# Optimization experiments

Hardware: AMD Instinct MI355X
Metric: run time of the kernel (lower is better)

## Reference

```python
import jax, jax.numpy as jnp
import numpy as np
import math

B, N, E, H = 32, 2000, 128, 8
D = E // H
NEG = -1e9
LN_EPS = 1e-5

def setup_inputs() -> dict:
    key = jax.random.key(0)
    ks = jax.random.split(key, 20)
    s = 1.0 / math.sqrt(E)
    inp = {
        'decoder_state': jax.random.normal(ks[0], (B, E), jnp.float32),
        'node_embeddings': jax.random.normal(ks[1], (B, N, E), jnp.float32),
        'mask': jax.random.randint(ks[2], (B, N), 0, 2, jnp.int32),
        'edge_weights': jax.random.uniform(ks[3], (B, N, N), jnp.float32),
        'visited': jax.random.randint(ks[4], (B, N), 0, 2).astype(bool),
        'prev_node': jax.random.randint(ks[5], (B,), 0, N, jnp.int64 if jax.config.jax_enable_x64 else jnp.int32),
        'all_visited': jax.random.randint(ks[6], (B,), 0, 2).astype(bool),
        'Wq': jax.random.uniform(ks[7], (E, E), jnp.float32, -s, s),
        'bq': jnp.zeros((E,), jnp.float32),
        'Wk': jax.random.uniform(ks[8], (E, E), jnp.float32, -s, s),
        'bk': jnp.zeros((E,), jnp.float32),
        'Wv': jax.random.uniform(ks[9], (E, E), jnp.float32, -s, s),
        'bv': jnp.zeros((E,), jnp.float32),
        'Wo': jax.random.uniform(ks[10], (E, E), jnp.float32, -s, s),
        'bo': jnp.zeros((E,), jnp.float32),
        'Wp': jax.random.uniform(ks[11], (E, E), jnp.float32, -s, s),
        'bp': jnp.zeros((E,), jnp.float32),
        'ln_g': jnp.ones((E,), jnp.float32),
        'ln_b': jnp.zeros((E,), jnp.float32),
        'shortcut_bonus': jnp.float32(5.0),
        'revisit_penalty': jnp.float32(-0.5),
    }
    return inp

def _forward(decoder_state, node_embeddings, edge_weights, Wq, bq, Wk, bk, Wv, bv, Wo, bo, Wp, bp, ln_g, ln_b, shortcut_bonus, revisit_penalty, mask, visited, prev_node, all_visited):
    # single-query MHA: q [B,1,E], kv [B,N,E]
    q = (decoder_state @ Wq + bq).reshape(B, H, 1, D)            # q_len=1
    k = (node_embeddings @ Wk + bk).reshape(B, N, H, D).transpose(0, 2, 1, 3)
    v = (node_embeddings @ Wv + bv).reshape(B, N, H, D).transpose(0, 2, 1, 3)
    att = jnp.einsum('bhqd,bhkd->bhqk', q, k) / math.sqrt(D)     # [B,H,1,N]
    att = jnp.where(mask[:, None, None, :] == 0, NEG, att)
    w = jax.nn.softmax(att, axis=-1)
    ctx = jnp.einsum('bhqk,bhkd->bhqd', w, v).transpose(0, 2, 1, 3).reshape(B, E)
    ctx = ctx @ Wo + bo
    # dropout in eval mode = identity; LayerNorm
    mu = jnp.mean(ctx, axis=-1, keepdims=True)
    var = jnp.mean((ctx - mu) ** 2, axis=-1, keepdims=True)
    nrm = (ctx - mu) / jnp.sqrt(var + LN_EPS) * ln_g + ln_b
    logits = nrm @ Wp + bp                                        # [B,E]
    scores = jnp.einsum('be,bne->bn', logits, node_embeddings)    # [B,N]
    # vectorized per-batch loop semantics
    not_all = ~all_visited                                        # [B]
    scores = jnp.where(not_all[:, None] & visited, revisit_penalty, scores)
    bidx = jnp.arange(B)
    direct = edge_weights[bidx, prev_node, 0]                     # [B]
    via = edge_weights[bidx, prev_node, :] + edge_weights[:, :, 0]  # [B,N]
    sav = (direct[:, None] - via) / direct[:, None]
    bonus = jnp.where(all_visited[:, None] & (via < direct[:, None]), shortcut_bonus * sav, 0.0)
    return scores + bonus

def reference(decoder_state, node_embeddings, mask, edge_weights, visited, prev_node, all_visited, Wq, bq, Wk, bk, Wv, bv, Wo, bo, Wp, bp, ln_g, ln_b, shortcut_bonus, revisit_penalty):
    return _forward(decoder_state, node_embeddings, edge_weights, Wq, bq, Wk, bk, Wv, bv, Wo, bo, Wp, bp, ln_g, ln_b, shortcut_bonus, revisit_penalty, mask, visited, prev_node, all_visited)
```

## Files before the change

kernel.cpp:

```cpp
#include <hip/hip_runtime.h>
#include <cstddef>

#define BB 32
#define NN 2000
#define EE 128
#define HH 8
#define DD 16
#define NCH 32
#define CHN 64
#define NEGV (-1e9f)

typedef __attribute__((ext_vector_type(8))) short short8v;
typedef __attribute__((ext_vector_type(4))) float f32x4;

__device__ __forceinline__ short f2bf(float f) {
  unsigned u = __float_as_uint(f);
  unsigned r = (u + 0x7FFFu + ((u >> 16) & 1u)) >> 16;
  return (short)r;
}
__device__ __forceinline__ float bf2f(short s) {
  return __uint_as_float(((unsigned)(unsigned short)s) << 16);
}


__global__ __launch_bounds__(256) void k_fused(
    const float* __restrict__ ds, const float* __restrict__ ne, const int* __restrict__ mask,
    const float* __restrict__ Wq, const float* __restrict__ bq,
    const float* __restrict__ Wk, const float* __restrict__ bk,
    short* __restrict__ pctx, float* __restrict__ pm, float* __restrict__ ps) {
  const int cpair = blockIdx.x, b = blockIdx.y, t = threadIdx.x;

  __shared__ float ds_s[EE], q_s[EE];
  __shared__ float redq[256];
  __shared__ __align__(16) short qk_sub[16 * EE];
  __shared__ float qbk_s[HH];
  __shared__ __align__(16) short ne_sub[CHN * EE];
  __shared__ __align__(16) short wT[16 * 72];
  __shared__ float att_s[HH * 66];
  __shared__ int mask_s[CHN];

  const int baseA = (2 * cpair) * CHN;
  const int baseB = baseA + CHN;
  const int cntB = (NN - baseB < CHN) ? (NN - baseB) : CHN;
  const int nrow = t >> 4, oct = t & 15;

  float4 pA[8];
#pragma unroll
  for (int i = 0; i < 4; ++i) {
    const int n = i * 16 + nrow;
    const float4* sA = (const float4*)(ne + ((size_t)b * NN + baseA + n) * EE + oct * 8);
    pA[2 * i] = sA[0]; pA[2 * i + 1] = sA[1];
  }
  int maskA_r = 0;
  if (t < CHN) maskA_r = mask[b * NN + baseA + t];
  if (t < EE) ds_s[t] = ds[b * EE + t];
  __builtin_amdgcn_sched_barrier(0);
  __syncthreads();

  const int o = t & 127, half = t >> 7;
  {
    const int c0 = half * 64;
    float a0 = 0.f, a1 = 0.f, a2 = 0.f, a3 = 0.f;
    for (int c = c0; c < c0 + 64; c += 4) {
      a0 = fmaf(ds_s[c],     Wq[(c)     * EE + o], a0);
      a1 = fmaf(ds_s[c + 1], Wq[(c + 1) * EE + o], a1);
      a2 = fmaf(ds_s[c + 2], Wq[(c + 2) * EE + o], a2);
      a3 = fmaf(ds_s[c + 3], Wq[(c + 3) * EE + o], a3);
    }
    redq[t] = (a0 + a1) + (a2 + a3);
  }
  __syncthreads();
  if (t < 128) q_s[t] = bq[t] + redq[t] + redq[t + 128];
  __syncthreads();

#pragma unroll
  for (int k = 0; k < 4; ++k) {
    const int f = t + k * 256;
    const int h = f >> 7, e = f & 127;
    const float4* wk4 = (const float4*)(Wk + e * EE + h * DD);
    const float4* q4 = (const float4*)(q_s + h * DD);
    float s = 0.f;
#pragma unroll
    for (int i = 0; i < 4; ++i) {
      const float4 w = wk4[i], q = q4[i];
      s += w.x * q.x + w.y * q.y + w.z * q.z + w.w * q.w;
    }
    qk_sub[((e >> 4) * 4 + (h >> 2)) * 64 + (h & 3) * 16 + (e & 15)] = f2bf(s);
  }
  for (int f = t; f < 512; f += 256) {
    const int eb = f >> 6, r = f & 63;
    ((int*)(qk_sub + eb * 256 + 128))[r] = 0;
  }
  if (t < HH) {
    float s = 0.f;
#pragma unroll
    for (int d = 0; d < DD; ++d) s += q_s[t * DD + d] * bk[t * DD + d];
    qbk_s[t] = s;
  }
  for (int f = t; f < 288; f += 256) ((int*)(wT + 8 * 72))[f] = 0;

  if (t < CHN) mask_s[t] = maskA_r;
#pragma unroll
  for (int i = 0; i < 4; ++i) {
    const int n = i * 16 + nrow;
    short8v s8;
    s8[0] = f2bf(pA[2 * i].x);     s8[1] = f2bf(pA[2 * i].y);
    s8[2] = f2bf(pA[2 * i].z);     s8[3] = f2bf(pA[2 * i].w);
    s8[4] = f2bf(pA[2 * i + 1].x); s8[5] = f2bf(pA[2 * i + 1].y);
    s8[6] = f2bf(pA[2 * i + 1].z); s8[7] = f2bf(pA[2 * i + 1].w);
    *(short8v*)(ne_sub + ((oct >> 1) * 16 + (n >> 2)) * 64 + (n & 3) * 16 + (oct & 1) * 8) = s8;
  }

  float4 pB[8];
#pragma unroll
  for (int i = 0; i < 4; ++i) {
    const int n = i * 16 + nrow;
    if (n < cntB) {
      const float4* sB = (const float4*)(ne + ((size_t)b * NN + baseB + n) * EE + oct * 8);
      pB[2 * i] = sB[0]; pB[2 * i + 1] = sB[1];
    } else {
      pB[2 * i] = make_float4(0.f, 0.f, 0.f, 0.f);
      pB[2 * i + 1] = make_float4(0.f, 0.f, 0.f, 0.f);
    }
  }
  int maskB_r = 0;
  if (t < CHN) maskB_r = (t < cntB) ? mask[b * NN + baseB + t] : 0;
  __builtin_amdgcn_sched_barrier(0);
  __syncthreads();

  const int w = t >> 6;
  const int l = t & 63;
  const int g = l >> 4;
  const int l15 = l & 15;

#pragma unroll 1
  for (int cc = 0; cc < 2; ++cc) {
    const int ci = 2 * cpair + cc;

    {
      f32x4 qacc = {0.f, 0.f, 0.f, 0.f};
      const int rn = w * 16 + l15;
#pragma unroll
      for (int ks = 0; ks < 4; ++ks) {
        const int eb = ks * 2 + (g >> 1), elo = (g & 1) * 8;
        short8v a = *(const short8v*)(qk_sub + (eb * 4 + (l15 >> 2)) * 64 + (l15 & 3) * 16 + elo);
        short8v bb = *(const short8v*)(ne_sub + (eb * 16 + (rn >> 2)) * 64 + (rn & 3) * 16 + elo);
        qacc = __builtin_amdgcn_mfma_f32_16x16x32_bf16(a, bb, qacc, 0, 0, 0);
      }
      if (g < 2) {
#pragma unroll
        for (int r = 0; r < 4; ++r) {
          const int h = g * 4 + r;
          att_s[h * 66 + rn] = mask_s[rn] ? (qacc[r] + qbk_s[h]) * 0.25f : NEGV;
        }
      }
    }
    __syncthreads();

    {
      const int h = t >> 5, l32 = t & 31;
      const float a0 = att_s[h * 66 + l32], a1 = att_s[h * 66 + l32 + 32];
      float mx = fmaxf(a0, a1);
#pragma unroll
      for (int k = 16; k >= 1; k >>= 1) mx = fmaxf(mx, __shfl_xor(mx, k, 32));
      const float w0 = mask_s[l32] ? expf(a0 - mx) : 0.f;
      const float w1 = mask_s[l32 + 32] ? expf(a1 - mx) : 0.f;
      const short s0 = f2bf(w0), s1 = f2bf(w1);
      float sm = bf2f(s0) + bf2f(s1);
#pragma unroll
      for (int k = 16; k >= 1; k >>= 1) sm += __shfl_xor(sm, k, 32);
      wT[h * 72 + l32] = s0;
      wT[h * 72 + l32 + 32] = s1;
      if (l32 == 0) {
        pm[(b * NCH + ci) * HH + h] = mx;
        ps[(b * NCH + ci) * HH + h] = sm;
      }
    }
    __syncthreads();

    {
      f32x4 pacc0 = {0.f, 0.f, 0.f, 0.f}, pacc1 = {0.f, 0.f, 0.f, 0.f};
#pragma unroll
      for (int ks = 0; ks < 2; ++ks) {
        short8v a = *(const short8v*)(wT + l15 * 72 + ks * 32 + g * 8);
#pragma unroll
        for (int ti = 0; ti < 2; ++ti) {
          const int e = (2 * w + ti) * 16 + l15;
          short8v bb;
#pragma unroll
          for (int j = 0; j < 8; ++j) {
            const int n = ks * 32 + g * 8 + j;
            bb[j] = ne_sub[((e >> 4) * 16 + (n >> 2)) * 64 + (n & 3) * 16 + (e & 15)];
          }
          if (ti == 0) pacc0 = __builtin_amdgcn_mfma_f32_16x16x32_bf16(a, bb, pacc0, 0, 0, 0);
          else         pacc1 = __builtin_amdgcn_mfma_f32_16x16x32_bf16(a, bb, pacc1, 0, 0, 0);
        }
      }
      if (g < 2) {
        short* dst = pctx + ((size_t)(b * NCH + ci) * HH) * EE;
#pragma unroll
        for (int r = 0; r < 4; ++r) {
          const int h = g * 4 + r;
          dst[h * EE + (2 * w) * 16 + l15]     = f2bf(pacc0[r]);
          dst[h * EE + (2 * w + 1) * 16 + l15] = f2bf(pacc1[r]);
        }
      }
    }

    if (cc == 0) {
      __syncthreads();
      if (t < CHN) mask_s[t] = maskB_r;
#pragma unroll
      for (int i = 0; i < 4; ++i) {
        const int n = i * 16 + nrow;
        short8v s8;
        s8[0] = f2bf(pB[2 * i].x);     s8[1] = f2bf(pB[2 * i].y);
        s8[2] = f2bf(pB[2 * i].z);     s8[3] = f2bf(pB[2 * i].w);
        s8[4] = f2bf(pB[2 * i + 1].x); s8[5] = f2bf(pB[2 * i + 1].y);
        s8[6] = f2bf(pB[2 * i + 1].z); s8[7] = f2bf(pB[2 * i + 1].w);
        *(short8v*)(ne_sub + ((oct >> 1) * 16 + (n >> 2)) * 64 + (n & 3) * 16 + (oct & 1) * 8) = s8;
      }
      __syncthreads();
    }
  }
}

__global__ __launch_bounds__(256) void k_head_scores(
    const float* __restrict__ ne,
    const short* __restrict__ pctx, const float* __restrict__ pm, const float* __restrict__ ps,
    const float* __restrict__ Wv, const float* __restrict__ bv,
    const float* __restrict__ Wo, const float* __restrict__ bo,
    const float* __restrict__ Wp, const float* __restrict__ bp,
    const float* __restrict__ ln_g, const float* __restrict__ ln_b,
    const int* __restrict__ visited, const int* __restrict__ prev_node,
    const int* __restrict__ all_visited, const float* __restrict__ ew,
    const float* __restrict__ sb_p, const float* __restrict__ rp_p,
    float* __restrict__ out) {
  const int x = blockIdx.x, b = blockIdx.y, t = threadIdx.x;
  __shared__ float mg_s[HH], dn_s[HH];
  __shared__ float sc_s[NCH * HH];
  __shared__ float cE[HH * EE];
  __shared__ float buf[EE];
  __shared__ float red[128];
  __shared__ float lg_s[EE];

  const int g = t >> 5, l = t & 31;
  const int nb = x * 125;
  float4 pref[16];
#pragma unroll
  for (int i = 0; i < 16; ++i) {
    const int nl = i * 8 + g;
    const int n = nb + ((nl < 125) ? nl : 0);
    pref[i] = *(const float4*)(ne + ((size_t)b * NN + n) * EE + l * 4);
  }
  __builtin_amdgcn_sched_barrier(0);

  if (t < HH) {
    float m = -INFINITY;
    for (int c = 0; c < NCH; ++c) m = fmaxf(m, pm[(b * NCH + c) * HH + t]);
    float dn = 0.f;
    for (int c = 0; c < NCH; ++c) dn += expf(pm[(b * NCH + c) * HH + t] - m) * ps[(b * NCH + c) * HH + t];
    mg_s[t] = m; dn_s[t] = dn;
  }
  __syncthreads();
  {
    const int c = t >> 3, hh = t & 7;
    sc_s[t] = expf(pm[(b * NCH + c) * HH + hh] - mg_s[hh]) / dn_s[hh];
  }
  __syncthreads();
  for (int f = t; f < HH * EE; f += 256) {
    const int hh = f >> 7, e = f & 127;
    float s = 0.f;
#pragma unroll 4
    for (int c = 0; c < NCH; ++c)
      s += sc_s[c * HH + hh] * bf2f(pctx[((size_t)(b * NCH + c) * HH + hh) * EE + e]);
    cE[f] = s;
  }
  __syncthreads();
  float acc2 = 0.f;
  if (t < 128) {
    float acc = bv[t];
    const int hh2 = t >> 4;
    for (int e = 0; e < EE; ++e) acc = fmaf(cE[hh2 * EE + e], Wv[e * EE + t], acc);
    buf[t] = acc;
  }
  __syncthreads();
  if (t < 128) {
    acc2 = bo[t];
    for (int e = 0; e < EE; ++e) acc2 = fmaf(buf[e], Wo[e * EE + t], acc2);
    red[t] = acc2;
  }
  __syncthreads();
  for (int s = 64; s > 0; s >>= 1) { if (t < s) red[t] += red[t + s]; __syncthreads(); }
  const float mu = red[0] / EE;
  __syncthreads();
  if (t < 128) red[t] = (acc2 - mu) * (acc2 - mu);
  __syncthreads();
  for (int s = 64; s > 0; s >>= 1) { if (t < s) red[t] += red[t + s]; __syncthreads(); }
  const float rstd = rsqrtf(red[0] / EE + 1e-5f);
  __syncthreads();
  if (t < 128) buf[t] = (acc2 - mu) * rstd * ln_g[t] + ln_b[t];
  __syncthreads();
  if (t < 128) {
    float acc3 = bp[t];
    for (int e = 0; e < EE; ++e) acc3 = fmaf(buf[e], Wp[e * EE + t], acc3);
    lg_s[t] = acc3;
  }
  __syncthreads();

  const float4 lg = *(const float4*)(lg_s + l * 4);
  const bool av = all_visited[b] != 0;
  const int pv = prev_node[b];
  const float direct = av ? ew[((size_t)b * NN + pv) * NN] : 1.f;
  const float sbv = sb_p[0], rpv = rp_p[0];
#pragma unroll
  for (int i = 0; i < 16; ++i) {
    const int nl = i * 8 + g;
    if (nl < 125) {
      const int n = nb + nl;
      const float4 a = pref[i];
      float d = a.x * lg.x + a.y * lg.y + a.z * lg.z + a.w * lg.w;
#pragma unroll
      for (int k = 16; k >= 1; k >>= 1) d += __shfl_xor(d, k, 32);
      if (l == 0) {
        float sc = d;
        if (!av) {
          if (visited[b * NN + n] != 0) sc = rpv;
        } else {
          const float via = ew[((size_t)b * NN + pv) * NN + n] + ew[((size_t)b * NN + n) * NN];
          if (via < direct) sc += sbv * (direct - via) / direct;
        }
        out[b * NN + n] = sc;
      }
    }
  }
}

extern "C" void kernel_launch(void* const* d_in, const int* in_sizes, int n_in,
                              void* d_out, int out_size, void* d_ws, size_t ws_size,
                              hipStream_t stream) {
  const float* ds   = (const float*)d_in[0];
  const float* ne   = (const float*)d_in[1];
  const int*   mask = (const int*)d_in[2];
  const float* ew   = (const float*)d_in[3];
  const int*   visited = (const int*)d_in[4];
  const int*   prev = (const int*)d_in[5];
  const int*   allv = (const int*)d_in[6];
  const float* Wq = (const float*)d_in[7];
  const float* bq = (const float*)d_in[8];
  const float* Wk = (const float*)d_in[9];
  const float* bk = (const float*)d_in[10];
  const float* Wv = (const float*)d_in[11];
  const float* bv = (const float*)d_in[12];
  const float* Wo = (const float*)d_in[13];
  const float* bo = (const float*)d_in[14];
  const float* Wp = (const float*)d_in[15];
  const float* bp = (const float*)d_in[16];
  const float* ln_g = (const float*)d_in[17];
  const float* ln_b = (const float*)d_in[18];
  const float* sb = (const float*)d_in[19];
  const float* rp = (const float*)d_in[20];
  float* out = (float*)d_out;
  char* ws = (char*)d_ws;

  short* pctx = (short*)ws;
  float* pm   = (float*)(ws + 2097152);
  float* ps   = (float*)(ws + 2129920);

  k_fused<<<dim3(16, BB), 256, 0, stream>>>(ds, ne, mask, Wq, bq, Wk, bk, pctx, pm, ps);
  k_head_scores<<<dim3(16, BB), 256, 0, stream>>>(ne, pctx, pm, ps, Wv, bv, Wo, bo, Wp, bp,
                                                  ln_g, ln_b, visited, prev, allv, ew, sb, rp, out);
}
```

Measured before the change: 53.41 us.

## Split head GEMVs across all 256 threads and double head-scores grid

```diff
diff --git a/kernel.cpp b/kernel.cpp
--- a/kernel.cpp
+++ b/kernel.cpp
@@ -240,17 +240,19 @@
   __shared__ float mg_s[HH], dn_s[HH];
   __shared__ float sc_s[NCH * HH];
   __shared__ float cE[HH * EE];
-  __shared__ float buf[EE];
-  __shared__ float red[128];
+  __shared__ float bufB[EE];
+  __shared__ float ctxo[EE];
+  __shared__ float redB[256];
   __shared__ float lg_s[EE];
 
   const int g = t >> 5, l = t & 31;
-  const int nb = x * 125;
-  float4 pref[16];
-#pragma unroll
-  for (int i = 0; i < 16; ++i) {
+  const int nb = x * 63;
+  const int cntS = (NN - nb < 63) ? (NN - nb) : 63;
+  float4 pref[8];
+#pragma unroll
+  for (int i = 0; i < 8; ++i) {
     const int nl = i * 8 + g;
-    const int n = nb + ((nl < 125) ? nl : 0);
+    const int n = nb + ((nl < cntS) ? nl : 0);
     pref[i] = *(const float4*)(ne + ((size_t)b * NN + n) * EE + l * 4);
   }
   __builtin_amdgcn_sched_barrier(0);
@@ -277,35 +279,48 @@
     cE[f] = s;
   }
   __syncthreads();
-  float acc2 = 0.f;
-  if (t < 128) {
-    float acc = bv[t];
-    const int hh2 = t >> 4;
-    for (int e = 0; e < EE; ++e) acc = fmaf(cE[hh2 * EE + e], Wv[e * EE + t], acc);
-    buf[t] = acc;
-  }
-  __syncthreads();
-  if (t < 128) {
-    acc2 = bo[t];
-    for (int e = 0; e < EE; ++e) acc2 = fmaf(buf[e], Wo[e * EE + t], acc2);
-    red[t] = acc2;
-  }
-  __syncthreads();
-  for (int s = 64; s > 0; s >>= 1) { if (t < s) red[t] += red[t + s]; __syncthreads(); }
-  const float mu = red[0] / EE;
-  __syncthreads();
-  if (t < 128) red[t] = (acc2 - mu) * (acc2 - mu);
-  __syncthreads();
-  for (int s = 64; s > 0; s >>= 1) { if (t < s) red[t] += red[t + s]; __syncthreads(); }
-  const float rstd = rsqrtf(red[0] / EE + 1e-5f);
-  __syncthreads();
-  if (t < 128) buf[t] = (acc2 - mu) * rstd * ln_g[t] + ln_b[t];
-  __syncthreads();
-  if (t < 128) {
-    float acc3 = bp[t];
-    for (int e = 0; e < EE; ++e) acc3 = fmaf(buf[e], Wp[e * EE + t], acc3);
-    lg_s[t] = acc3;
-  }
+
+  const int o = t & 127, half = t >> 7;
+  const int e0 = half * 64;
+  {
+    const int hh2 = o >> 4;
+    float acc = 0.f;
+#pragma unroll 4
+    for (int e = e0; e < e0 + 64; ++e) acc = fmaf(cE[hh2 * EE + e], Wv[e * EE + o], acc);
+    redB[t] = acc;
+  }
+  __syncthreads();
+  if (t < 128) bufB[t] = bv[t] + redB[t] + redB[t + 128];
+  __syncthreads();
+  {
+    float acc = 0.f;
+#pragma unroll 4
+    for (int e = e0; e < e0 + 64; ++e) acc = fmaf(bufB[e], Wo[e * EE + o], acc);
+    redB[t] = acc;
+  }
+  __syncthreads();
+  if (t < 128) ctxo[t] = bo[t] + redB[t] + redB[t + 128];
+  __syncthreads();
+  if (t < 128) redB[t] = ctxo[t];
+  __syncthreads();
+  for (int s = 64; s > 0; s >>= 1) { if (t < s) redB[t] += redB[t + s]; __syncthreads(); }
+  const float mu = redB[0] / EE;
+  __syncthreads();
+  if (t < 128) redB[t] = (ctxo[t] - mu) * (ctxo[t] - mu);
+  __syncthreads();
+  for (int s = 64; s > 0; s >>= 1) { if (t < s) redB[t] += redB[t + s]; __syncthreads(); }
+  const float rstd = rsqrtf(redB[0] / EE + 1e-5f);
+  __syncthreads();
+  if (t < 128) bufB[t] = (ctxo[t] - mu) * rstd * ln_g[t] + ln_b[t];
+  __syncthreads();
+  {
+    float acc = 0.f;
+#pragma unroll 4
+    for (int e = e0; e < e0 + 64; ++e) acc = fmaf(bufB[e], Wp[e * EE + o], acc);
+    redB[t] = acc;
+  }
+  __syncthreads();
+  if (t < 128) lg_s[t] = bp[t] + redB[t] + redB[t + 128];
   __syncthreads();
 
   const float4 lg = *(const float4*)(lg_s + l * 4);
@@ -314,9 +329,9 @@
   const float direct = av ? ew[((size_t)b * NN + pv) * NN] : 1.f;
   const float sbv = sb_p[0], rpv = rp_p[0];
 #pragma unroll
-  for (int i = 0; i < 16; ++i) {
+  for (int i = 0; i < 8; ++i) {
     const int nl = i * 8 + g;
-    if (nl < 125) {
+    if (nl < cntS) {
       const int n = nb + nl;
       const float4 a = pref[i];
       float d = a.x * lg.x + a.y * lg.y + a.z * lg.z + a.w * lg.w;
@@ -368,6 +383,6 @@
   float* ps   = (float*)(ws + 2129920);
 
   k_fused<<<dim3(16, BB), 256, 0, stream>>>(ds, ne, mask, Wq, bq, Wk, bk, pctx, pm, ps);
-  k_head_scores<<<dim3(16, BB), 256, 0, stream>>>(ne, pctx, pm, ps, Wv, bv, Wo, bo, Wp, bp,
+  k_head_scores<<<dim3(32, BB), 256, 0, stream>>>(ne, pctx, pm, ps, Wv, bv, Wo, bo, Wp, bp,
                                                   ln_g, ln_b, visited, prev, allv, ew, sb, rp, out);
 }
```

Result: slower. 56.93 us (+6.6%).
